# Optimization experiments

Measured on AMD Instinct MI355X. Metric: run time of the kernel, lower is better.

## Reference

```python
import jax, jax.numpy as jnp
import numpy as np

DIM = 512
HEADS = 4
DIM_HEAD = 64          # dim // 8
INNER = HEADS * DIM_HEAD  # 256
M_LANDMARKS = 256      # dim // 2
PINV_ITERS = 6
KS = 33                # residual_conv_kernel
LN_EPS = 1e-5


def setup_inputs() -> dict:
    key = jax.random.key(0)
    ks = jax.random.split(key, 6)
    B, N = 8, 4096
    x = jax.random.normal(ks[0], (B, N, DIM), dtype=jnp.float32)
    ln_g = jnp.ones((DIM,), jnp.float32)
    ln_b = jnp.zeros((DIM,), jnp.float32)
    w_qkv = jax.random.normal(ks[1], (DIM, 3 * INNER), jnp.float32) * 0.02
    w_out = jax.random.normal(ks[2], (INNER, DIM), jnp.float32) * 0.02
    b_out = jnp.zeros((DIM,), jnp.float32)
    # depthwise Conv2d(heads, heads, (33,1), groups=heads, bias=False): OIHW = (4,1,33,1)
    w_res = jax.random.normal(ks[3], (HEADS, 1, KS, 1), jnp.float32) * 0.05
    return dict(x=x, ln_g=ln_g, ln_b=ln_b, w_qkv=w_qkv, w_out=w_out, b_out=b_out, w_res=w_res)


def moore_penrose_pinv(x, iters=PINV_ITERS):
    # x: [B, H, m, m]
    abs_x = jnp.abs(x)
    col = abs_x.sum(-1)
    row = abs_x.sum(-2)
    z = jnp.swapaxes(x, -1, -2) / (jnp.max(col) * jnp.max(row))
    I = jnp.eye(x.shape[-1], dtype=x.dtype)
    for _ in range(iters):
        xz = x @ z
        z = 0.25 * z @ (13. * I - xz @ (15. * I - xz @ (7. * I - xz)))
    return z


def reference(x, ln_g, ln_b, w_qkv, w_out, b_out, w_res):
    B, N, D = x.shape
    h, dh, m = HEADS, DIM_HEAD, M_LANDMARKS
    l = N // m  # landmark group size (N chosen divisible by m, so no padding)

    # pre-norm LayerNorm
    mu = x.mean(-1, keepdims=True)
    var = ((x - mu) ** 2).mean(-1, keepdims=True)
    xn = (x - mu) / jnp.sqrt(var + LN_EPS) * ln_g + ln_b

    qkv = xn @ w_qkv  # [B, N, 3*INNER]
    q, k, v = jnp.split(qkv, 3, axis=-1)
    to_heads = lambda t: t.reshape(B, N, h, dh).transpose(0, 2, 1, 3)  # [B,h,N,dh]
    q, k, v = to_heads(q), to_heads(k), to_heads(v)
    q = q * (dh ** -0.5)

    # landmarks: mean over contiguous groups of l  ('b h (n l) d -> b h n d')
    q_l = q.reshape(B, h, m, l, dh).mean(3)  # [B,h,m,dh]
    k_l = k.reshape(B, h, m, l, dh).mean(3)

    sim1 = jnp.einsum('bhid,bhjd->bhij', q, k_l)    # [B,h,N,m]
    sim2 = jnp.einsum('bhid,bhjd->bhij', q_l, k_l)  # [B,h,m,m]
    sim3 = jnp.einsum('bhid,bhjd->bhij', q_l, k)    # [B,h,m,N]

    a1 = jax.nn.softmax(sim1, axis=-1)
    a2 = jax.nn.softmax(sim2, axis=-1)
    a3 = jax.nn.softmax(sim3, axis=-1)

    a2_inv = moore_penrose_pinv(a2)
    out = (a1 @ a2_inv) @ (a3 @ v)  # [B,h,N,dh]

    # residual depthwise conv on v along sequence: treat as NCHW with C=h, H=N, W=dh
    conv = jax.lax.conv_general_dilated(
        v, w_res, window_strides=(1, 1),
        padding=((KS // 2, KS // 2), (0, 0)),
        feature_group_count=h,
        dimension_numbers=('NCHW', 'OIHW', 'NCHW'))
    out = out + conv

    out = out.transpose(0, 2, 1, 3).reshape(B, N, h * dh)
    out = out @ w_out + b_out  # to_out (dropout=0.1 inactive in eval)
    return x + out
```

## Files before the change

kernel.cpp:

```cpp
#include <hip/hip_runtime.h>
#include <hip/hip_bf16.h>
#include <string.h>

typedef __hip_bfloat16 bf16;
typedef __attribute__((ext_vector_type(8))) __bf16 bf16x8;
typedef __attribute__((ext_vector_type(4))) float f32x4;
typedef __attribute__((ext_vector_type(8))) unsigned short u16x8;

#define NN 4096
#define DD 512
#define MM 256
#define ROWS 32768

__device__ __forceinline__ float b2f(bf16 x) { return __bfloat162float(x); }
__device__ __forceinline__ float u2f(unsigned short u) {
  return __uint_as_float(((unsigned int)u) << 16);
}
__device__ __forceinline__ unsigned short f2bu(float v) {
  bf16 h = __float2bfloat16(v);
  return *reinterpret_cast<unsigned short*>(&h);
}
__device__ __forceinline__ float ldf(const void* p, size_t i, int f) {
  return f ? ((const float*)p)[i] : __bfloat162float(((const bf16*)p)[i]);
}
__device__ __forceinline__ void stf(void* p, size_t i, float v, int f) {
  if (f) ((float*)p)[i] = v;
  else ((bf16*)p)[i] = __float2bfloat16(v);
}

__global__ void detect_kernel(const void* x, int* flag) {
  __shared__ int red[256];
  int tid = threadIdx.x;
  const unsigned short* u = (const unsigned short*)x;
  int local = 0;
  for (int i = 0; i < 32; i++) {
    unsigned short e = (u[tid * 32 + i] >> 7) & 0xFF;
    if (e >= 0xC8) local++;
  }
  red[tid] = local; __syncthreads();
  #pragma unroll
  for (int s = 128; s > 0; s >>= 1) {
    if (tid < s) red[tid] += red[tid + s];
    __syncthreads();
  }
  if (tid == 0) *flag = (red[0] > 32) ? 1 : 0;
}

__device__ __forceinline__ float bred_max(float v, float* red) {
  int tid = threadIdx.x;
  red[tid] = v; __syncthreads();
  #pragma unroll
  for (int s = 128; s > 0; s >>= 1) {
    if (tid < s) red[tid] = fmaxf(red[tid], red[tid + s]);
    __syncthreads();
  }
  float r = red[0]; __syncthreads();
  return r;
}
__device__ __forceinline__ float bred_sum(float v, float* red) {
  int tid = threadIdx.x;
  red[tid] = v; __syncthreads();
  #pragma unroll
  for (int s = 128; s > 0; s >>= 1) {
    if (tid < s) red[tid] += red[tid + s];
    __syncthreads();
  }
  float r = red[0]; __syncthreads();
  return r;
}

__global__ void ln_stats_kernel(const void* __restrict__ x, float* __restrict__ stats,
                                const int* dflag) {
  __shared__ float red[256];
  int f = *dflag;
  int row = blockIdx.x, tid = threadIdx.x;
  size_t base = (size_t)row * DD;
  float v0 = ldf(x, base + tid, f);
  float v1 = ldf(x, base + tid + 256, f);
  float mean = bred_sum(v0 + v1, red) * (1.0f / DD);
  float d0 = v0 - mean, d1 = v1 - mean;
  float var = bred_sum(d0 * d0 + d1 * d1, red) * (1.0f / DD);
  if (tid == 0) {
    stats[row * 2] = mean;
    stats[row * 2 + 1] = rsqrtf(var + 1e-5f);
  }
}

__global__ void transpose_kernel(const void* __restrict__ in, bf16* __restrict__ out,
                                 int R, int Cc, long sIn, long sOut,
                                 const int* dflag, int ovr) {
  int f = (ovr >= 0) ? ovr : *dflag;
  size_t o = (size_t)blockIdx.x * 256 + threadIdx.x;
  size_t per = (size_t)R * Cc;
  size_t b = o / per, rem = o % per;
  size_t c = rem / R, r = rem % R;
  out[b * sOut + c * (size_t)R + r] = __float2bfloat16(ldf(in, b * sIn + r * (size_t)Cc + c, f));
}

__global__ __launch_bounds__(256) void gemm_qkv(
    const void* __restrict__ x, const float* __restrict__ stats,
    const void* __restrict__ g, const void* __restrict__ bb,
    const bf16* __restrict__ wT,
    bf16* __restrict__ q, bf16* __restrict__ k, bf16* __restrict__ v,
    const int* __restrict__ dflag) {
  __shared__ __align__(16) unsigned short As[128][40];
  __shared__ __align__(16) unsigned short Bs[128][40];
  __shared__ __align__(16) float gls[512];
  __shared__ __align__(16) float bls[512];
  int f = *dflag;
  int tid = threadIdx.x;
  {
    int c0 = tid, c1 = tid + 256;
    gls[c0] = ldf(g, c0, f);  gls[c1] = ldf(g, c1, f);
    bls[c0] = ldf(bb, c0, f); bls[c1] = ldf(bb, c1, f);
  }
  int m0 = blockIdx.x * 128, n0 = blockIdx.y * 128;
  int sr = tid >> 1, sh = (tid & 1) * 16;
  int wave = tid >> 6, lane = tid & 63;
  int wm = (wave & 1) * 64, wn = (wave >> 1) * 64;
  int l15 = lane & 15, quad = lane >> 4;
  int r = m0 + sr;
  float mu = stats[r * 2], rs = stats[r * 2 + 1];
  const float* xf = (const float*)x + (size_t)r * DD;
  const bf16*  xb = (const bf16*)x  + (size_t)r * DD;
  __syncthreads();
  f32x4 acc[4][4] = {};
  for (int k0 = 0; k0 < 512; k0 += 32) {
    {
      float xv[16];
      if (f) {
        const float* src = xf + k0 + sh;
        float4 t0 = *(const float4*)(src);
        float4 t1 = *(const float4*)(src + 4);
        float4 t2 = *(const float4*)(src + 8);
        float4 t3 = *(const float4*)(src + 12);
        xv[0] = t0.x; xv[1] = t0.y; xv[2]  = t0.z; xv[3]  = t0.w;
        xv[4] = t1.x; xv[5] = t1.y; xv[6]  = t1.z; xv[7]  = t1.w;
        xv[8] = t2.x; xv[9] = t2.y; xv[10] = t2.z; xv[11] = t2.w;
        xv[12] = t3.x; xv[13] = t3.y; xv[14] = t3.z; xv[15] = t3.w;
      } else {
        const bf16* src = xb + k0 + sh;
        u16x8 t0 = *(const u16x8*)(src);
        u16x8 t1 = *(const u16x8*)(src + 8);
        #pragma unroll
        for (int e = 0; e < 8; e++) { xv[e] = u2f(t0[e]); xv[8 + e] = u2f(t1[e]); }
      }
      float gv[16], bv[16];
      {
        const float* gp = &gls[k0 + sh];
        const float* bp = &bls[k0 + sh];
        #pragma unroll
        for (int e4 = 0; e4 < 4; e4++) {
          float4 gt = *(const float4*)(gp + e4 * 4);
          float4 bt = *(const float4*)(bp + e4 * 4);
          gv[e4 * 4 + 0] = gt.x; gv[e4 * 4 + 1] = gt.y; gv[e4 * 4 + 2] = gt.z; gv[e4 * 4 + 3] = gt.w;
          bv[e4 * 4 + 0] = bt.x; bv[e4 * 4 + 1] = bt.y; bv[e4 * 4 + 2] = bt.z; bv[e4 * 4 + 3] = bt.w;
        }
      }
      u16x8 w0, w1;
      #pragma unroll
      for (int e = 0; e < 8; e++) {
        float a0 = rs * gv[e];
        float a1 = rs * gv[e + 8];
        w0[e] = f2bu(xv[e] * a0 + (bv[e] - mu * a0));
        w1[e] = f2bu(xv[e + 8] * a1 + (bv[e + 8] - mu * a1));
      }
      *(u16x8*)&As[sr][sh] = w0;
      *(u16x8*)&As[sr][sh + 8] = w1;
    }
    {
      const bf16* src = wT + (size_t)(n0 + sr) * 512 + k0 + sh;
      *(u16x8*)&Bs[sr][sh] = *(const u16x8*)src;
      *(u16x8*)&Bs[sr][sh + 8] = *(const u16x8*)(src + 8);
    }
    __syncthreads();
    bf16x8 af[4], bfr[4];
    #pragma unroll
    for (int i = 0; i < 4; i++) af[i] = *(const bf16x8*)&As[wm + i * 16 + l15][quad * 8];
    #pragma unroll
    for (int j = 0; j < 4; j++) bfr[j] = *(const bf16x8*)&Bs[wn + j * 16 + l15][quad * 8];
    #pragma unroll
    for (int i = 0; i < 4; i++)
      #pragma unroll
      for (int j = 0; j < 4; j++)
        acc[i][j] = __builtin_amdgcn_mfma_f32_16x16x32_bf16(af[i], bfr[j], acc[i][j], 0, 0, 0);
    __syncthreads();
  }
  #pragma unroll
  for (int i = 0; i < 4; i++)
    #pragma unroll
    for (int j = 0; j < 4; j++)
      #pragma unroll
      for (int reg = 0; reg < 4; reg++) {
        int row = m0 + wm + i * 16 + quad * 4 + reg;
        int c = n0 + wn + j * 16 + l15;
        int which = c >> 8, within = c & 255, h = within >> 6, d = within & 63;
        int b_ = row >> 12, n = row & 4095;
        size_t idx = ((size_t)(b_ * 4 + h) * NN + n) * 64 + d;
        float val = acc[i][j][reg];
        if (which == 0) q[idx] = __float2bfloat16(val * 0.125f);
        else if (which == 1) k[idx] = __float2bfloat16(val);
        else v[idx] = __float2bfloat16(val);
      }
}

__global__ __launch_bounds__(256) void gemm_bt(
    const bf16* __restrict__ A, long ldA, long sA,
    const bf16* __restrict__ Bt, long ldB, long sB,
    void* __restrict__ C, long ldC, long sC,
    int N, int kLen, int nTiles, int mode,
    const void* __restrict__ bias, const void* __restrict__ resid,
    const int* __restrict__ dflag) {
  __shared__ __align__(16) unsigned short As[128][40];
  __shared__ __align__(16) unsigned short Bs[128][40];
  int tid = threadIdx.x;
  int b = blockIdx.x;
  int m0 = blockIdx.y * 128;
  int nt = blockIdx.z % nTiles, ks = blockIdx.z / nTiles;
  int n0 = nt * 128;
  long k0b = (long)ks * kLen;
  const bf16* Ab = A + (size_t)b * sA;
  const bf16* Bb = Bt + (size_t)b * sB;
  int sr = tid >> 1, sh = (tid & 1) * 16;
  int wave = tid >> 6, lane = tid & 63;
  int wm = (wave & 1) * 64, wn = (wave >> 1) * 64;
  int l15 = lane & 15, quad = lane >> 4;
  f32x4 acc[4][4] = {};
  for (int kc = 0; kc < kLen; kc += 32) {
    long k0 = k0b + kc;
    {
      const bf16* src = Ab + (size_t)(m0 + sr) * ldA + k0 + sh;
      *(u16x8*)&As[sr][sh] = *(const u16x8*)src;
      *(u16x8*)&As[sr][sh + 8] = *(const u16x8*)(src + 8);
    }
    if (n0 + sr < N) {
      const bf16* src = Bb + (size_t)(n0 + sr) * ldB + k0 + sh;
      *(u16x8*)&Bs[sr][sh] = *(const u16x8*)src;
      *(u16x8*)&Bs[sr][sh + 8] = *(const u16x8*)(src + 8);
    } else {
      u16x8 z = {};
      *(u16x8*)&Bs[sr][sh] = z;
      *(u16x8*)&Bs[sr][sh + 8] = z;
    }
    __syncthreads();
    bf16x8 af[4], bfr[4];
    #pragma unroll
    for (int i = 0; i < 4; i++) af[i] = *(const bf16x8*)&As[wm + i * 16 + l15][quad * 8];
    #pragma unroll
    for (int j = 0; j < 4; j++) bfr[j] = *(const bf16x8*)&Bs[wn + j * 16 + l15][quad * 8];
    #pragma unroll
    for (int i = 0; i < 4; i++)
      #pragma unroll
      for (int j = 0; j < 4; j++)
        acc[i][j] = __builtin_amdgcn_mfma_f32_16x16x32_bf16(af[i], bfr[j], acc[i][j], 0, 0, 0);
    __syncthreads();
  }
  int f = (mode == 3) ? *dflag : 0;
  #pragma unroll
  for (int i = 0; i < 4; i++)
    #pragma unroll
    for (int j = 0; j < 4; j++)
      #pragma unroll
      for (int reg = 0; reg < 4; reg++) {
        int row = m0 + wm + i * 16 + quad * 4 + reg;
        int col = n0 + wn + j * 16 + l15;
        if (col < N) {
          float val = acc[i][j][reg];
          size_t off = (size_t)row * ldC + col;
          if (mode == 0) (((float*)C) + (size_t)b * sC)[off] = val;
          else if (mode == 1) (((bf16*)C) + (size_t)b * sC)[off] = __float2bfloat16(val);
          else if (mode == 2) atomicAdd(((float*)C) + (size_t)b * sC + off, val);
          else {
            val += ldf(bias, col, f) + ldf(resid, off, f);
            stf(C, off, val, f);
          }
        }
      }
}

__global__ void landmark_kernel(const bf16* __restrict__ src, float* __restrict__ dstf,
                                bf16* __restrict__ dstb) {
  int idx = blockIdx.x * 256 + threadIdx.x;
  int d = idx & 63, j = (idx >> 6) & 255, bh = idx >> 14;
  const bf16* s = src + ((size_t)bh * NN + j * 16) * 64 + d;
  float a = 0;
  #pragma unroll
  for (int i = 0; i < 16; i++) a += b2f(s[i * 64]);
  a *= (1.0f / 16);
  dstf[idx] = a;
  dstb[idx] = __float2bfloat16(a);
}

__global__ void a2_kernel(const float* __restrict__ ql, const float* __restrict__ kl,
                          float* __restrict__ a2) {
  __shared__ float qs[64];
  __shared__ float red[256];
  int bh = blockIdx.x >> 8, i = blockIdx.x & 255, tid = threadIdx.x;
  if (tid < 64) qs[tid] = ql[((size_t)bh * MM + i) * 64 + tid];
  __syncthreads();
  const float* kr = kl + ((size_t)bh * MM + tid) * 64;
  float s = 0;
  #pragma unroll
  for (int d = 0; d < 64; d++) s += qs[d] * kr[d];
  float mx = bred_max(s, red);
  float e = __expf(s - mx);
  float sm = bred_sum(e, red);
  a2[((size_t)bh * MM + i) * MM + tid] = e / sm;
}

__global__ void colsum_max_kernel(const float* __restrict__ a2, float* __restrict__ gmax) {
  __shared__ float red[256];
  int bh = blockIdx.x, tid = threadIdx.x;
  const float* base = a2 + (size_t)bh * MM * MM + tid;
  float s0 = 0, s1 = 0, s2 = 0, s3 = 0, s4 = 0, s5 = 0, s6 = 0, s7 = 0;
  for (int i = 0; i < 256; i += 8) {
    s0 += base[(size_t)(i + 0) * MM];
    s1 += base[(size_t)(i + 1) * MM];
    s2 += base[(size_t)(i + 2) * MM];
    s3 += base[(size_t)(i + 3) * MM];
    s4 += base[(size_t)(i + 4) * MM];
    s5 += base[(size_t)(i + 5) * MM];
    s6 += base[(size_t)(i + 6) * MM];
    s7 += base[(size_t)(i + 7) * MM];
  }
  float tot = ((s0 + s1) + (s2 + s3)) + ((s4 + s5) + (s6 + s7));
  float mx = bred_max(tot, red);
  if (tid == 0) atomicMax((int*)gmax + 1, __float_as_int(mx));
}

__global__ void zinit_kernel(const float* __restrict__ a2, const float* __restrict__ gmax,
                             float* __restrict__ z) {
  int idx = blockIdx.x * 256 + threadIdx.x;
  int j = idx & 255, i = (idx >> 8) & 255, bh = idx >> 16;
  float scale = 1.0f / gmax[1];
  z[idx] = a2[((size_t)bh * MM + j) * MM + i] * scale;
}

__global__ __launch_bounds__(256) void bmm64_mfma(
    const float* __restrict__ A, const float* __restrict__ B_,
    float* __restrict__ C,
    int Nn, int Kk, long sA, long sB, long sC,
    float alpha, float beta, float gbA, float gbB) {
  __shared__ __align__(16) unsigned short Ah[64][40];
  __shared__ __align__(16) unsigned short Al[64][40];
  __shared__ __align__(16) unsigned short Bh[64][40];
  __shared__ __align__(16) unsigned short Bl[64][40];
  int bh = blockIdx.x;
  int row0 = blockIdx.y * 64, col0 = blockIdx.z * 64;
  const float* Ab = A + (size_t)bh * sA;
  const float* Bb = B_ + (size_t)bh * sB;
  int tid = threadIdx.x;
  int wave = tid >> 6, lane = tid & 63, l15 = lane & 15, quad = lane >> 4;
  int wm = (wave & 1) * 32, wn = (wave >> 1) * 32;
  int ar2 = tid >> 2, kq = (tid & 3) * 8;
  int kr = tid >> 3, n8 = (tid & 7) * 8;
  f32x4 acc[2][2] = {};
  for (int k0 = 0; k0 < Kk; k0 += 32) {
    {
      const float* src = Ab + (size_t)(row0 + ar2) * Kk + k0 + kq;
      u16x8 hi, lo;
      #pragma unroll
      for (int e = 0; e < 8; e++) {
        float a = src[e];
        unsigned short h = f2bu(a);
        hi[e] = h;
        lo[e] = f2bu(a - u2f(h));
      }
      *(u16x8*)&Ah[ar2][kq] = hi;
      *(u16x8*)&Al[ar2][kq] = lo;
    }
    {
      const float* src = Bb + (size_t)(k0 + kr) * Nn + col0 + n8;
      int kk = k0 + kr;
      #pragma unroll
      for (int e = 0; e < 8; e++) {
        float b = gbB * src[e];
        if (kk == col0 + n8 + e) b += gbA;
        unsigned short h = f2bu(b);
        Bh[n8 + e][kr] = h;
        Bl[n8 + e][kr] = f2bu(b - u2f(h));
      }
    }
    __syncthreads();
    bf16x8 ah[2], al[2], bhf[2], blf[2];
    #pragma unroll
    for (int i = 0; i < 2; i++) {
      ah[i]  = *(const bf16x8*)&Ah[wm + i * 16 + l15][quad * 8];
      al[i]  = *(const bf16x8*)&Al[wm + i * 16 + l15][quad * 8];
      bhf[i] = *(const bf16x8*)&Bh[wn + i * 16 + l15][quad * 8];
      blf[i] = *(const bf16x8*)&Bl[wn + i * 16 + l15][quad * 8];
    }
    #pragma unroll
    for (int i = 0; i < 2; i++)
      #pragma unroll
      for (int j = 0; j < 2; j++) {
        acc[i][j] = __builtin_amdgcn_mfma_f32_16x16x32_bf16(ah[i], bhf[j], acc[i][j], 0, 0, 0);
        acc[i][j] = __builtin_amdgcn_mfma_f32_16x16x32_bf16(ah[i], blf[j], acc[i][j], 0, 0, 0);
        acc[i][j] = __builtin_amdgcn_mfma_f32_16x16x32_bf16(al[i], bhf[j], acc[i][j], 0, 0, 0);
      }
    __syncthreads();
  }
  #pragma unroll
  for (int i = 0; i < 2; i++)
    #pragma unroll
    for (int j = 0; j < 2; j++)
      #pragma unroll
      for (int reg = 0; reg < 4; reg++) {
        int r = row0 + wm + i * 16 + quad * 4 + reg;
        int cc = col0 + wn + j * 16 + l15;
        C[(size_t)bh * sC + (size_t)r * Nn + cc] = alpha * (r == cc) + beta * acc[i][j][reg];
      }
}

__global__ void wmsplit_kernel(const float* __restrict__ Wm, bf16* __restrict__ h,
                               bf16* __restrict__ l) {
  int o = blockIdx.x * 256 + threadIdx.x;
  int c = o & 255, d = (o >> 8) & 63, bh = o >> 14;
  float w = Wm[(((size_t)bh << 8) + c) * 64 + d];
  unsigned short hh = f2bu(w);
  h[o] = __float2bfloat16(w);
  l[o] = __float2bfloat16(w - u2f(hh));
}

__global__ __launch_bounds__(512) void sim3_flash_kernel(
    const bf16* __restrict__ qlbf, const bf16* __restrict__ k,
    const bf16* __restrict__ vT, float* __restrict__ a3v) {
  __shared__ __align__(16) unsigned short Qs[32][72];
  __shared__ __align__(16) unsigned short Pl[8][32][72];
  __shared__ __align__(16) float OW[32][64];
  __shared__ float mW[8][32];
  __shared__ float lW[8][32];
  int tid = threadIdx.x;
  int lt = blockIdx.x;
  int bh = blockIdx.y;
  int lm0 = lt * 32;
  if (tid < 256) {
    int r = tid >> 3, s = (tid & 7) * 8;
    *(u16x8*)&Qs[r][s] = *(const u16x8*)(qlbf + ((size_t)bh * 256 + lm0 + r) * 64 + s);
  }
  {
    float4 z = {};
    ((float4*)OW)[tid] = z;
  }
  __syncthreads();
  int wid = tid >> 6, lane = tid & 63, l15 = lane & 15, quad = lane >> 4;
  const bf16* kb = k + (size_t)bh * (NN * 64);
  const bf16* vb = vT + (size_t)bh * 262144;
  unsigned short* Pw = &Pl[wid][0][0];
  float m_[2] = {-1e30f, -1e30f};
  float l_[2] = {0.f, 0.f};
  f32x4 acc_o[2][4] = {};
  for (int ch = 0; ch < 8; ch++) {
    int kvb = wid * 512 + ch * 64;
    f32x4 acc_s[4][2] = {};
    #pragma unroll
    for (int kc = 0; kc < 2; kc++) {
      bf16x8 kf[4], qf[2];
      #pragma unroll
      for (int i = 0; i < 4; i++)
        kf[i] = *(const bf16x8*)(kb + (size_t)(kvb + i * 16 + l15) * 64 + kc * 32 + quad * 8);
      #pragma unroll
      for (int j = 0; j < 2; j++)
        qf[j] = *(const bf16x8*)&Qs[j * 16 + l15][kc * 32 + quad * 8];
      #pragma unroll
      for (int i = 0; i < 4; i++)
        #pragma unroll
        for (int j = 0; j < 2; j++)
          acc_s[i][j] = __builtin_amdgcn_mfma_f32_16x16x32_bf16(kf[i], qf[j], acc_s[i][j], 0, 0, 0);
    }
    float scl[2];
    #pragma unroll
    for (int js = 0; js < 2; js++) {
      float cm = acc_s[0][js][0];
      #pragma unroll
      for (int i = 0; i < 4; i++)
        #pragma unroll
        for (int reg = 0; reg < 4; reg++) cm = fmaxf(cm, acc_s[i][js][reg]);
      cm = fmaxf(cm, __shfl_xor(cm, 16));
      cm = fmaxf(cm, __shfl_xor(cm, 32));
      float mn = fmaxf(m_[js], cm);
      scl[js] = __expf(m_[js] - mn);
      m_[js] = mn;
    }
    #pragma unroll
    for (int io = 0; io < 2; io++)
      #pragma unroll
      for (int reg = 0; reg < 4; reg++) {
        float sb = __shfl(scl[io], quad * 4 + reg);
        #pragma unroll
        for (int jd = 0; jd < 4; jd++) acc_o[io][jd][reg] *= sb;
      }
    #pragma unroll
    for (int js = 0; js < 2; js++) {
      float cs = 0;
      #pragma unroll
      for (int i = 0; i < 4; i++)
        #pragma unroll
        for (int reg = 0; reg < 4; reg++) {
          float p = __expf(acc_s[i][js][reg] - m_[js]);
          cs += p;
          Pw[(js * 16 + l15) * 72 + i * 16 + quad * 4 + reg] = f2bu(p);
        }
      cs += __shfl_xor(cs, 16);
      cs += __shfl_xor(cs, 32);
      l_[js] = l_[js] * scl[js] + cs;
    }
    #pragma unroll
    for (int kc2 = 0; kc2 < 2; kc2++) {
      bf16x8 pf[2], vf[4];
      #pragma unroll
      for (int io = 0; io < 2; io++)
        pf[io] = *(const bf16x8*)&Pw[(io * 16 + l15) * 72 + kc2 * 32 + quad * 8];
      #pragma unroll
      for (int jd = 0; jd < 4; jd++)
        vf[jd] = *(const bf16x8*)(vb + (size_t)(jd * 16 + l15) * 4096 + kvb + kc2 * 32 + quad * 8);
      #pragma unroll
      for (int io = 0; io < 2; io++)
        #pragma unroll
        for (int jd = 0; jd < 4; jd++)
          acc_o[io][jd] = __builtin_amdgcn_mfma_f32_16x16x32_bf16(pf[io], vf[jd], acc_o[io][jd], 0, 0, 0);
    }
  }
  if (quad == 0) {
    mW[wid][l15] = m_[0]; mW[wid][16 + l15] = m_[1];
    lW[wid][l15] = l_[0]; lW[wid][16 + l15] = l_[1];
  }
  __syncthreads();
  #pragma unroll
  for (int io = 0; io < 2; io++)
    #pragma unroll
    for (int reg = 0; reg < 4; reg++) {
      int lm = io * 16 + quad * 4 + reg;
      float ms = mW[0][lm];
      #pragma unroll
      for (int w = 1; w < 8; w++) ms = fmaxf(ms, mW[w][lm]);
      float ls = 0;
      #pragma unroll
      for (int w = 0; w < 8; w++) ls += __expf(mW[w][lm] - ms) * lW[w][lm];
      float fac = __expf(mW[wid][lm] - ms) / ls;
      #pragma unroll
      for (int jd = 0; jd < 4; jd++)
        atomicAdd(&OW[lm][jd * 16 + l15], acc_o[io][jd][reg] * fac);
    }
  __syncthreads();
  {
    float4 o = ((float4*)OW)[tid];
    *(float4*)(a3v + (size_t)bh * 16384 + (size_t)lm0 * 64 + tid * 4) = o;
  }
}

__global__ __launch_bounds__(256) void attn1_pv_kernel(
    const bf16* __restrict__ q, const bf16* __restrict__ klbf,
    const bf16* __restrict__ wmt_h, const bf16* __restrict__ wmt_l,
    float* __restrict__ p1f, int bh0) {
  __shared__ __align__(16) unsigned short Qs[32][72];
  __shared__ __align__(16) unsigned short Ks[256][72];
  __shared__ __align__(16) unsigned short Wh[64][40];
  __shared__ __align__(16) unsigned short Wl[64][40];
  __shared__ float redm[4][32];
  __shared__ float reds[4][32];
  int tid = threadIdx.x;
  int bhl = blockIdx.y, bh = bh0 + bhl;
  int n0 = blockIdx.x * 32;
  const bf16* qb = q + ((size_t)bh * NN + n0) * 64;
  const bf16* kb = klbf + (size_t)bh * 16384;
  {
    int r = tid >> 3, s = (tid & 7) * 8;
    *(u16x8*)&Qs[r][s] = *(const u16x8*)(qb + (size_t)r * 64 + s);
  }
  {
    const bf16* src = kb + (size_t)tid * 64;
    #pragma unroll
    for (int s8 = 0; s8 < 8; s8++) *(u16x8*)&Ks[tid][s8 * 8] = *(const u16x8*)(src + s8 * 8);
  }
  __syncthreads();
  int wave = tid >> 6, lane = tid & 63, l15 = lane & 15, quad = lane >> 4;
  f32x4 acc[2][4] = {};
  #pragma unroll
  for (int kc = 0; kc < 64; kc += 32) {
    bf16x8 af[2], bfr[4];
    #pragma unroll
    for (int i = 0; i < 2; i++) af[i] = *(const bf16x8*)&Qs[i * 16 + l15][kc + quad * 8];
    #pragma unroll
    for (int j = 0; j < 4; j++) bfr[j] = *(const bf16x8*)&Ks[wave * 64 + j * 16 + l15][kc + quad * 8];
    #pragma unroll
    for (int i = 0; i < 2; i++)
      #pragma unroll
      for (int j = 0; j < 4; j++)
        acc[i][j] = __builtin_amdgcn_mfma_f32_16x16x32_bf16(af[i], bfr[j], acc[i][j], 0, 0, 0);
  }
  float lm[2][4], ls[2][4], rinv[2][4];
  #pragma unroll
  for (int i = 0; i < 2; i++)
    #pragma unroll
    for (int reg = 0; reg < 4; reg++)
      lm[i][reg] = fmaxf(fmaxf(acc[i][0][reg], acc[i][1][reg]),
                         fmaxf(acc[i][2][reg], acc[i][3][reg]));
  #pragma unroll
  for (int off = 1; off < 16; off <<= 1)
    #pragma unroll
    for (int i = 0; i < 2; i++)
      #pragma unroll
      for (int reg = 0; reg < 4; reg++) lm[i][reg] = fmaxf(lm[i][reg], __shfl_xor(lm[i][reg], off));
  if (l15 == 0)
    #pragma unroll
    for (int i = 0; i < 2; i++)
      #pragma unroll
      for (int reg = 0; reg < 4; reg++) redm[wave][i * 16 + quad * 4 + reg] = lm[i][reg];
  __syncthreads();
  #pragma unroll
  for (int i = 0; i < 2; i++)
    #pragma unroll
    for (int reg = 0; reg < 4; reg++) {
      int r = i * 16 + quad * 4 + reg;
      rinv[i][reg] = fmaxf(fmaxf(redm[0][r], redm[1][r]), fmaxf(redm[2][r], redm[3][r]));
      ls[i][reg] = 0;
    }
  #pragma unroll
  for (int i = 0; i < 2; i++)
    #pragma unroll
    for (int j = 0; j < 4; j++)
      #pragma unroll
      for (int reg = 0; reg < 4; reg++) {
        float e = __expf(acc[i][j][reg] - rinv[i][reg]);
        acc[i][j][reg] = e;
        ls[i][reg] += e;
      }
  #pragma unroll
  for (int off = 1; off < 16; off <<= 1)
    #pragma unroll
    for (int i = 0; i < 2; i++)
      #pragma unroll
      for (int reg = 0; reg < 4; reg++) ls[i][reg] += __shfl_xor(ls[i][reg], off);
  if (l15 == 0)
    #pragma unroll
    for (int i = 0; i < 2; i++)
      #pragma unroll
      for (int reg = 0; reg < 4; reg++) reds[wave][i * 16 + quad * 4 + reg] = ls[i][reg];
  __syncthreads();
  #pragma unroll
  for (int i = 0; i < 2; i++)
    #pragma unroll
    for (int reg = 0; reg < 4; reg++) {
      int r = i * 16 + quad * 4 + reg;
      rinv[i][reg] = 1.0f / (reds[0][r] + reds[1][r] + reds[2][r] + reds[3][r]);
    }
  unsigned short* Pb = &Ks[0][0];
  #pragma unroll
  for (int i = 0; i < 2; i++)
    #pragma unroll
    for (int j = 0; j < 4; j++)
      #pragma unroll
      for (int reg = 0; reg < 4; reg++) {
        float pv = acc[i][j][reg] * rinv[i][reg];
        unsigned short h = f2bu(pv);
        int row = i * 16 + quad * 4 + reg;
        int col = wave * 64 + j * 16 + l15;
        Pb[row * 264 + col] = h;
        Pb[8448 + row * 264 + col] = f2bu(pv - u2f(h));
      }
  const bf16* whp = wmt_h + (size_t)bh * 16384;
  const bf16* wlp = wmt_l + (size_t)bh * 16384;
  int wd = tid >> 2, wc = (tid & 3) * 8;
  int iw = wave & 1, dw = (wave >> 1) * 32;
  f32x4 accp[2] = {};
  for (int kc = 0; kc < 256; kc += 32) {
    __syncthreads();
    *(u16x8*)&Wh[wd][wc] = *(const u16x8*)(whp + (size_t)wd * 256 + kc + wc);
    *(u16x8*)&Wl[wd][wc] = *(const u16x8*)(wlp + (size_t)wd * 256 + kc + wc);
    __syncthreads();
    bf16x8 ah = *(const bf16x8*)&Pb[(iw * 16 + l15) * 264 + kc + quad * 8];
    bf16x8 al = *(const bf16x8*)&Pb[8448 + (iw * 16 + l15) * 264 + kc + quad * 8];
    #pragma unroll
    for (int jj = 0; jj < 2; jj++) {
      bf16x8 bh2 = *(const bf16x8*)&Wh[dw + jj * 16 + l15][quad * 8];
      bf16x8 bl2 = *(const bf16x8*)&Wl[dw + jj * 16 + l15][quad * 8];
      accp[jj] = __builtin_amdgcn_mfma_f32_16x16x32_bf16(ah, bh2, accp[jj], 0, 0, 0);
      accp[jj] = __builtin_amdgcn_mfma_f32_16x16x32_bf16(ah, bl2, accp[jj], 0, 0, 0);
      accp[jj] = __builtin_amdgcn_mfma_f32_16x16x32_bf16(al, bh2, accp[jj], 0, 0, 0);
    }
  }
  #pragma unroll
  for (int jj = 0; jj < 2; jj++)
    #pragma unroll
    for (int reg = 0; reg < 4; reg++) {
      int r = iw * 16 + quad * 4 + reg;
      int d = dw + jj * 16 + l15;
      int n = n0 + r;
      p1f[((size_t)bhl * NN + n) * 64 + d] = accp[jj][reg];
    }
}

__global__ __launch_bounds__(256) void conv_add_kernel(
    const float* __restrict__ p1, const bf16* __restrict__ v,
    const void* __restrict__ wres, bf16* __restrict__ y, const int* __restrict__ dflag,
    int bh0) {
  __shared__ __align__(16) unsigned short Vs[96][64];
  int f = *dflag;
  int tid = threadIdx.x;
  int bhl = blockIdx.y, bh = bh0 + bhl;
  int n0 = blockIdx.x * 64;
  int h = bh & 3, b_ = bh >> 2;
  const bf16* vb = v + (size_t)bh * (NN * 64);
  for (int rr = tid; rr < 384; rr += 256) {
    int r = rr >> 2, s = (rr & 3) * 16;
    int n = n0 - 16 + r;
    if (n >= 0 && n < NN) {
      *(u16x8*)&Vs[r][s] = *(const u16x8*)(vb + (size_t)n * 64 + s);
      *(u16x8*)&Vs[r][s + 8] = *(const u16x8*)(vb + (size_t)n * 64 + s + 8);
    } else {
      u16x8 z = {};
      *(u16x8*)&Vs[r][s] = z; *(u16x8*)&Vs[r][s + 8] = z;
    }
  }
  float w33[33];
  #pragma unroll
  for (int kk = 0; kk < 33; kk++) w33[kk] = ldf(wres, h * 33 + kk, f);
  __syncthreads();
  int d = tid & 63, rb = tid >> 6;
  for (int ii = 0; ii < 16; ii++) {
    int nl = ii * 4 + rb;
    float cv = 0;
    #pragma unroll
    for (int kk = 0; kk < 33; kk++) cv += w33[kk] * u2f(Vs[nl + kk][d]);
    int n = n0 + nl;
    float pv = p1[((size_t)bhl * NN + n) * 64 + d];
    y[((size_t)b_ * NN + n) * 256 + h * 64 + d] = __float2bfloat16(pv + cv);
  }
}

extern "C" void kernel_launch(void* const* d_in, const int* in_sizes, int n_in,
                              void* d_out, int out_size, void* d_ws, size_t ws_size,
                              hipStream_t stream) {
  const void* x     = d_in[0];
  const void* ln_g  = d_in[1];
  const void* ln_b  = d_in[2];
  const void* w_qkv = d_in[3];
  const void* w_out = d_in[4];
  const void* b_out = d_in[5];
  const void* w_res = d_in[6];

  float* ws    = (float*)d_ws;
  float* gmax  = ws;
  int*   dflag = (int*)(ws + 2);
  float* stats = ws + 256;
  bf16*  woutT = (bf16*)(stats + 65536);
  float* qlf   = (float*)(stats + 65536 + 65536);
  float* klf   = qlf + 524288;
  bf16*  qlbf  = (bf16*)(klf + 524288);
  bf16*  klbf  = qlbf + 524288;
  float* a3v   = (float*)(klbf + 524288);
  float* Wm    = a3v + 524288;
  float* a2    = Wm + 524288;
  bf16*  q     = (bf16*)(a2 + 2097152);
  bf16*  k     = q + 8388608;
  bf16*  v     = k + 8388608;
  bf16*  y     = k;
  bf16*  wmt_h = (bf16*)a2;
  bf16*  wmt_l = wmt_h + 524288;

  char* dob = (char*)d_out;
  bf16* wqkvT = (bf16*)dob;
  bf16* vTfull = (bf16*)dob;
  float* W0   = (float*)dob;
  float* W1   = (float*)(dob + (8u << 20));
  float* W2   = (float*)(dob + (16u << 20));
  float* W3   = (float*)(dob + (24u << 20));
  float* p1f  = (float*)dob;

  detect_kernel<<<1, 256, 0, stream>>>(x, dflag);
  hipMemsetAsync(gmax, 0, 2 * sizeof(float), stream);
  ln_stats_kernel<<<ROWS, 256, 0, stream>>>(x, stats, dflag);

  transpose_kernel<<<1536, 256, 0, stream>>>(w_qkv, wqkvT, 512, 768, 0, 0, dflag, -1);
  transpose_kernel<<<512, 256, 0, stream>>>(w_out, woutT, 256, 512, 0, 0, dflag, -1);

  gemm_qkv<<<dim3(256, 6), 256, 0, stream>>>(x, stats, ln_g, ln_b, wqkvT, q, k, v, dflag);

  landmark_kernel<<<2048, 256, 0, stream>>>(q, qlf, qlbf);
  landmark_kernel<<<2048, 256, 0, stream>>>(k, klf, klbf);

  transpose_kernel<<<32768, 256, 0, stream>>>(v, vTfull, 4096, 64, 262144, 262144, dflag, 0);
  sim3_flash_kernel<<<dim3(8, 32), 512, 0, stream>>>(qlbf, k, vTfull, a3v);

  a2_kernel<<<8192, 256, 0, stream>>>(qlf, klf, a2);
  colsum_max_kernel<<<32, 256, 0, stream>>>(a2, gmax);
  zinit_kernel<<<8192, 256, 0, stream>>>(a2, gmax, W0);

  float* zi = W0; float* f1 = W1; float* f2 = W2; float* f3 = W3;
  for (int it = 0; it < 6; it++) {
    bmm64_mfma<<<dim3(32, 4, 4), 256, 0, stream>>>(a2, zi, f1, 256, 256, 65536, 65536, 65536, 0.f, 1.f, 0.f, 1.f);
    bmm64_mfma<<<dim3(32, 4, 4), 256, 0, stream>>>(f1, f1, f2, 256, 256, 65536, 65536, 65536, 15.f, -1.f, 7.f, -1.f);
    bmm64_mfma<<<dim3(32, 4, 4), 256, 0, stream>>>(f1, f2, f3, 256, 256, 65536, 65536, 65536, 13.f, -1.f, 0.f, 1.f);
    bmm64_mfma<<<dim3(32, 4, 4), 256, 0, stream>>>(zi, f3, f2, 256, 256, 65536, 65536, 65536, 0.f, 0.25f, 0.f, 1.f);
    float* nzi = f2; f2 = f1; f1 = zi; zi = nzi;
  }

  bmm64_mfma<<<dim3(32, 4, 1), 256, 0, stream>>>(zi, a3v, Wm, 64, 256, 65536, 16384, 16384, 0.f, 1.f, 0.f, 1.f);

  wmsplit_kernel<<<2048, 256, 0, stream>>>(Wm, wmt_h, wmt_l);

  attn1_pv_kernel<<<dim3(128, 32), 256, 0, stream>>>(q, klbf, wmt_h, wmt_l, p1f, 0);
  conv_add_kernel<<<dim3(64, 32), 256, 0, stream>>>(p1f, v, w_res, y, dflag, 0);

  gemm_bt<<<dim3(1, 256, 4), 256, 0, stream>>>(
      y, 256, 0, woutT, 256, 0,
      d_out, 512, 0, 512, 256, 4, 3, b_out, x, dflag);
}
```

Before: 903.8 us.

## Vectorize LN stats per wave and stage GEMM epilogues through LDS

LayerNorm stats now run one row per wavefront with vectorized 8-element loads and shuffle reductions in a single pass (sum and sum of squares), replacing a two-pass shared-memory tree reduction with one row per block. The QKV GEMM and the output GEMM (mode 3) epilogues now stage accumulators through shared memory so each thread writes 8 contiguous outputs as one 16-byte store, instead of scattered scalar stores. The bias and residual loads in the output GEMM are vectorized the same way. The one-pass variance formula is slightly less numerically robust, and the epilogues add extra barriers.

```diff
diff --git a/kernel.cpp b/kernel.cpp
--- a/kernel.cpp
+++ b/kernel.cpp
@@ -71,16 +71,34 @@
 
 __global__ void ln_stats_kernel(const void* __restrict__ x, float* __restrict__ stats,
                                 const int* dflag) {
-  __shared__ float red[256];
   int f = *dflag;
-  int row = blockIdx.x, tid = threadIdx.x;
-  size_t base = (size_t)row * DD;
-  float v0 = ldf(x, base + tid, f);
-  float v1 = ldf(x, base + tid + 256, f);
-  float mean = bred_sum(v0 + v1, red) * (1.0f / DD);
-  float d0 = v0 - mean, d1 = v1 - mean;
-  float var = bred_sum(d0 * d0 + d1 * d1, red) * (1.0f / DD);
-  if (tid == 0) {
+  int wave = threadIdx.x >> 6, lane = threadIdx.x & 63;
+  int row = blockIdx.x * 4 + wave;
+  size_t base = (size_t)row * DD + lane * 8;
+  float v[8];
+  if (f) {
+    const float* xp = (const float*)x + base;
+    float4 a = *(const float4*)xp;
+    float4 b = *(const float4*)(xp + 4);
+    v[0] = a.x; v[1] = a.y; v[2] = a.z; v[3] = a.w;
+    v[4] = b.x; v[5] = b.y; v[6] = b.z; v[7] = b.w;
+  } else {
+    const bf16* xp = (const bf16*)x + base;
+    u16x8 t = *(const u16x8*)xp;
+    #pragma unroll
+    for (int e = 0; e < 8; e++) v[e] = u2f(t[e]);
+  }
+  float s = 0, s2 = 0;
+  #pragma unroll
+  for (int e = 0; e < 8; e++) { s += v[e]; s2 += v[e] * v[e]; }
+  #pragma unroll
+  for (int off = 1; off < 64; off <<= 1) {
+    s += __shfl_xor(s, off);
+    s2 += __shfl_xor(s2, off);
+  }
+  if (lane == 0) {
+    float mean = s * (1.0f / DD);
+    float var = s2 * (1.0f / DD) - mean * mean;
     stats[row * 2] = mean;
     stats[row * 2 + 1] = rsqrtf(var + 1e-5f);
   }
@@ -186,22 +204,34 @@
         acc[i][j] = __builtin_amdgcn_mfma_f32_16x16x32_bf16(af[i], bfr[j], acc[i][j], 0, 0, 0);
     __syncthreads();
   }
-  #pragma unroll
-  for (int i = 0; i < 4; i++)
-    #pragma unroll
-    for (int j = 0; j < 4; j++)
-      #pragma unroll
-      for (int reg = 0; reg < 4; reg++) {
-        int row = m0 + wm + i * 16 + quad * 4 + reg;
-        int c = n0 + wn + j * 16 + l15;
-        int which = c >> 8, within = c & 255, h = within >> 6, d = within & 63;
-        int b_ = row >> 12, n = row & 4095;
-        size_t idx = ((size_t)(b_ * 4 + h) * NN + n) * 64 + d;
-        float val = acc[i][j][reg];
-        if (which == 0) q[idx] = __float2bfloat16(val * 0.125f);
-        else if (which == 1) k[idx] = __float2bfloat16(val);
-        else v[idx] = __float2bfloat16(val);
-      }
+  float* eps = (float*)&As[0][0];
+  int half = wave & 1;
+  int er = tid >> 4, ec8 = (tid & 15) * 8;
+  for (int p = 0; p < 8; p++) {
+    if (half == (p >> 2)) {
+      int i = p & 3;
+      #pragma unroll
+      for (int j = 0; j < 4; j++)
+        #pragma unroll
+        for (int reg = 0; reg < 4; reg++)
+          eps[(quad * 4 + reg) * 132 + wn + j * 16 + l15] = acc[i][j][reg];
+    }
+    __syncthreads();
+    {
+      int row = m0 + p * 16 + er;
+      int c = n0 + ec8;
+      int which = c >> 8, h = (c >> 6) & 3, d = c & 63;
+      int b_ = row >> 12, n = row & 4095;
+      const float* src = &eps[er * 132 + ec8];
+      float scale = (which == 0) ? 0.125f : 1.0f;
+      u16x8 o;
+      #pragma unroll
+      for (int e = 0; e < 8; e++) o[e] = f2bu(src[e] * scale);
+      bf16* dst = (which == 0) ? q : (which == 1) ? k : v;
+      *(u16x8*)(dst + ((size_t)(b_ * 4 + h) * NN + n) * 64 + d) = o;
+    }
+    __syncthreads();
+  }
 }
 
 __global__ __launch_bounds__(256) void gemm_bt(
@@ -255,7 +285,55 @@
         acc[i][j] = __builtin_amdgcn_mfma_f32_16x16x32_bf16(af[i], bfr[j], acc[i][j], 0, 0, 0);
     __syncthreads();
   }
-  int f = (mode == 3) ? *dflag : 0;
+  if (mode == 3) {
+    int f = *dflag;
+    float* eps = (float*)&As[0][0];
+    int half = wave & 1;
+    int er = tid >> 4, ec8 = (tid & 15) * 8;
+    int colb = n0 + ec8;
+    float bias8[8];
+    #pragma unroll
+    for (int e = 0; e < 8; e++) bias8[e] = ldf(bias, colb + e, f);
+    for (int p = 0; p < 8; p++) {
+      if (half == (p >> 2)) {
+        int i = p & 3;
+        #pragma unroll
+        for (int j = 0; j < 4; j++)
+          #pragma unroll
+          for (int reg = 0; reg < 4; reg++)
+            eps[(quad * 4 + reg) * 132 + wn + j * 16 + l15] = acc[i][j][reg];
+      }
+      __syncthreads();
+      {
+        int row = m0 + p * 16 + er;
+        size_t off = (size_t)row * ldC + colb;
+        const float* src = &eps[er * 132 + ec8];
+        if (f) {
+          float* Cp = (float*)C + off;
+          const float* xr = (const float*)resid + off;
+          float4 r0 = *(const float4*)xr;
+          float4 r1 = *(const float4*)(xr + 4);
+          float4 o0, o1;
+          o0.x = src[0] + bias8[0] + r0.x; o0.y = src[1] + bias8[1] + r0.y;
+          o0.z = src[2] + bias8[2] + r0.z; o0.w = src[3] + bias8[3] + r0.w;
+          o1.x = src[4] + bias8[4] + r1.x; o1.y = src[5] + bias8[5] + r1.y;
+          o1.z = src[6] + bias8[6] + r1.z; o1.w = src[7] + bias8[7] + r1.w;
+          *(float4*)Cp = o0;
+          *(float4*)(Cp + 4) = o1;
+        } else {
+          bf16* Cp = (bf16*)C + off;
+          const bf16* xr = (const bf16*)resid + off;
+          u16x8 rv = *(const u16x8*)xr;
+          u16x8 o;
+          #pragma unroll
+          for (int e = 0; e < 8; e++) o[e] = f2bu(src[e] + bias8[e] + u2f(rv[e]));
+          *(u16x8*)Cp = o;
+        }
+      }
+      __syncthreads();
+    }
+    return;
+  }
   #pragma unroll
   for (int i = 0; i < 4; i++)
     #pragma unroll
@@ -269,11 +347,7 @@
           size_t off = (size_t)row * ldC + col;
           if (mode == 0) (((float*)C) + (size_t)b * sC)[off] = val;
           else if (mode == 1) (((bf16*)C) + (size_t)b * sC)[off] = __float2bfloat16(val);
-          else if (mode == 2) atomicAdd(((float*)C) + (size_t)b * sC + off, val);
-          else {
-            val += ldf(bias, col, f) + ldf(resid, off, f);
-            stf(C, off, val, f);
-          }
+          else atomicAdd(((float*)C) + (size_t)b * sC + off, val);
         }
       }
 }
@@ -770,7 +844,7 @@
 
   detect_kernel<<<1, 256, 0, stream>>>(x, dflag);
   hipMemsetAsync(gmax, 0, 2 * sizeof(float), stream);
-  ln_stats_kernel<<<ROWS, 256, 0, stream>>>(x, stats, dflag);
+  ln_stats_kernel<<<8192, 256, 0, stream>>>(x, stats, dflag);
 
   transpose_kernel<<<1536, 256, 0, stream>>>(w_qkv, wqkvT, 512, 768, 0, 0, dflag, -1);
   transpose_kernel<<<512, 256, 0, stream>>>(w_out, woutT, 256, 512, 0, 0, dflag, -1);
```

After: 850.1 us. -5.9%, faster.
